# Kernel tuning notes

Measured on AMD Instinct MI355X. Metric: run time of the kernel, lower is better.

The kernel has to match this reference:

```python
import jax, jax.numpy as jnp
import numpy as np

B, Q, G = 32, 4000, 100
C1, C2, C3 = 4, 32, 8
ALPHA, GAMMA = 0.25, 2.0
OTA_K = 5
CENTER_RADIUS = 2.5
COST_BBOX = 1.0
COST_GIOU = 1.0
COST_CLASS = 1.0 / 3.0  # forward sets self.cost_class = 1/len(heads) = 1/3


def box_xyxy_to_cxcywh(b):
    x0, y0, x1, y1 = b[..., 0], b[..., 1], b[..., 2], b[..., 3]
    return jnp.stack([(x0 + x1) * 0.5, (y0 + y1) * 0.5, x1 - x0, y1 - y0], axis=-1)


def box_cxcywh_to_xyxy(b):
    cx, cy, w, h = b[..., 0], b[..., 1], b[..., 2], b[..., 3]
    return jnp.stack([cx - 0.5 * w, cy - 0.5 * h, cx + 0.5 * w, cy + 0.5 * h], axis=-1)


def box_iou(a, b):
    # a [Q,4], b [G,4] in xyxy -> iou, union [Q,G]
    area_a = (a[:, 2] - a[:, 0]) * (a[:, 3] - a[:, 1])
    area_b = (b[:, 2] - b[:, 0]) * (b[:, 3] - b[:, 1])
    lt = jnp.maximum(a[:, None, :2], b[None, :, :2])
    rb = jnp.minimum(a[:, None, 2:], b[None, :, 2:])
    wh = jnp.clip(rb - lt, 0.0)
    inter = wh[..., 0] * wh[..., 1]
    union = area_a[:, None] + area_b[None, :] - inter
    return inter / union, union


def generalized_box_iou(a, b):
    iou, union = box_iou(a, b)
    lt = jnp.minimum(a[:, None, :2], b[None, :, :2])
    rb = jnp.maximum(a[:, None, 2:], b[None, :, 2:])
    wh = jnp.clip(rb - lt, 0.0)
    area = wh[..., 0] * wh[..., 1]
    return iou - (area - union) / area


def get_in_boxes_info(boxes_c, gts_c):
    # boxes_c [Q,4] cxcywh anchors, gts_c [G,4] cxcywh gts
    xy = box_cxcywh_to_xyxy(gts_c)  # [G,4]
    ax, ay = boxes_c[:, 0:1], boxes_c[:, 1:2]  # [Q,1]
    in_box = (ax > xy[:, 0]) & (ax < xy[:, 2]) & (ay > xy[:, 1]) & (ay < xy[:, 3])  # [Q,G]
    w = xy[:, 2] - xy[:, 0]
    h = xy[:, 3] - xy[:, 1]
    cx, cy = gts_c[:, 0], gts_c[:, 1]
    in_ctr = ((ax > cx - CENTER_RADIUS * w) & (ax < cx + CENTER_RADIUS * w) &
              (ay > cy - CENTER_RADIUS * h) & (ay < cy + CENTER_RADIUS * h))
    fg_mask = jnp.any(in_box, axis=1) | jnp.any(in_ctr, axis=1)  # [Q]
    return fg_mask, in_box & in_ctr


def compute_cost(l1, l2, l3, pb, gb, isz, t1, t2, t3):
    fg_mask, in_bc = get_in_boxes_info(box_xyxy_to_cxcywh(pb), box_xyxy_to_cxcywh(gb))
    ious, _ = box_iou(pb, gb)

    def focal_cost(logits, labels):
        p = jax.nn.sigmoid(logits)
        neg = (1.0 - ALPHA) * p ** GAMMA * (-jnp.log(1.0 - p + 1e-8))
        pos = ALPHA * (1.0 - p) ** GAMMA * (-jnp.log(p + 1e-8))
        return (pos - neg)[:, labels]  # [Q,G]

    cc = focal_cost(l1, t1) + focal_cost(l2, t2) + focal_cost(l3, t3)
    nb = pb / isz[None, :]
    ng = gb / isz[None, :]
    cost_bbox = jnp.sum(jnp.abs(nb[:, None, :] - ng[None, :, :]), axis=-1)  # L1 cdist [Q,G]
    cost_giou = -generalized_box_iou(pb, gb)
    cost = (COST_BBOX * cost_bbox + COST_CLASS * cc + COST_GIOU * cost_giou
            + 100.0 * (~in_bc).astype(cost_bbox.dtype))
    cost = cost + 10000.0 * (~fg_mask)[:, None].astype(cost.dtype)
    return cost, ious


def dynamic_k_matching(cost, ious):
    q, g = cost.shape
    topk_ious, _ = jax.lax.top_k(ious.T, OTA_K)  # [G,k]
    dynamic_ks = jnp.clip(topk_ious.sum(1).astype(jnp.int32), 1, None)  # [G]
    # top dynamic_ks[g] lowest-cost queries per gt (dynamic_ks <= OTA_K since ious in [0,1])
    _, pos_idx = jax.lax.top_k(-cost.T, OTA_K)  # [G,k]
    valid = (jnp.arange(OTA_K)[None, :] < dynamic_ks[:, None]).astype(cost.dtype)
    m = jnp.zeros_like(cost).at[pos_idx, jnp.arange(g)[:, None]].add(valid)

    def resolve(m_, c_):
        # anchors matched to >1 gt keep only their min-cost gt
        multi = m_.sum(1) > 1
        one = jax.nn.one_hot(jnp.argmin(c_, axis=1), g, dtype=m_.dtype)
        return jnp.where(multi[:, None], one, m_)

    m = resolve(m, cost)

    def cond(st):
        return jnp.any(st[0].sum(0) == 0)

    def body(st):
        m_, c_ = st
        c_ = c_ + jnp.where((m_.sum(1) > 0)[:, None], 1e5, 0.0)  # penalize already-matched queries
        unmatched = m_.sum(0) == 0  # [G]
        one = jax.nn.one_hot(jnp.argmin(c_, axis=0), q, dtype=m_.dtype, axis=0)  # [Q,G]
        m_ = jnp.where(unmatched[None, :], one, m_)
        m_ = resolve(m_, c_)
        return (m_, c_)

    m, c = jax.lax.while_loop(cond, body, (m, cost))
    selected = m.sum(1) > 0            # [Q] bool: which queries are matched
    gt_idx = jnp.argmax(m, axis=1)     # [Q] gt index per query (valid where selected)
    matched_qidx = jnp.argmin(jnp.where(m > 0, c, jnp.inf), axis=0)  # [G]
    return m, selected, gt_idx, matched_qidx


def reference(pred_logits_1, pred_logits_2, pred_logits_3, pred_boxes, gt_boxes_xyxy, img_size, labels_1, labels_2, labels_3):
    def per_image(l1, l2, l3, pb, gb, isz, t1, t2, t3):
        cost, ious = compute_cost(l1, l2, l3, pb, gb, isz, t1, t2, t3)
        m, selected, gt_idx, matched_qidx = dynamic_k_matching(cost, ious)
        return m, selected, gt_idx, matched_qidx, cost
    return jax.vmap(per_image)(pred_logits_1, pred_logits_2, pred_logits_3,
                               pred_boxes, gt_boxes_xyxy, img_size,
                               labels_1, labels_2, labels_3)


def setup_inputs() -> dict:
    key = jax.random.key(0)
    ks = jax.random.split(key, 8)

    def rand_boxes(k, n):
        k1, k2 = jax.random.split(k)
        cxcy = jax.random.uniform(k1, (B, n, 2), minval=32.0, maxval=480.0)
        wh = jax.random.uniform(k2, (B, n, 2), minval=16.0, maxval=128.0)
        return jnp.concatenate([cxcy - wh * 0.5, cxcy + wh * 0.5], axis=-1)

    return {
        "pred_logits_1": jax.random.normal(ks[0], (B, Q, C1), jnp.float32),
        "pred_logits_2": jax.random.normal(ks[1], (B, Q, C2), jnp.float32),
        "pred_logits_3": jax.random.normal(ks[2], (B, Q, C3), jnp.float32),
        "pred_boxes": rand_boxes(ks[3], Q),
        "gt_boxes_xyxy": rand_boxes(ks[4], G),
        "img_size": jnp.full((B, 4), 512.0, jnp.float32),
        "labels_1": jax.random.randint(ks[5], (B, G), 0, C1),
        "labels_2": jax.random.randint(ks[6], (B, G), 0, C2),
        "labels_3": jax.random.randint(ks[7], (B, G), 0, C3),
    }
```

## Files before the change

### kernel.cpp

```cpp
#include <hip/hip_runtime.h>
#include <math.h>
#include <stdint.h>

#define NB 32
#define NQ 4000
#define NG 100
#define NC1 4
#define NC2 32
#define NC3 8
#define NCT 44
#define GCH 25
#define SLK 16

static const size_t OFF_M    = 0;
static const size_t OFF_SEL  = (size_t)NB * NQ * NG;
static const size_t OFF_GTI  = OFF_SEL + (size_t)NB * NQ;
static const size_t OFF_MQ   = OFF_GTI + (size_t)NB * NQ;
static const size_t OFF_COST = OFF_MQ + (size_t)NB * NG;

__device__ __forceinline__ float focal_diff(float x) {
    float p   = 1.0f / (1.0f + expf(-x));
    float neg = 0.75f * (p * p) * (-logf(1.0f - p + 1e-8f));
    float pos = 0.25f * ((1.0f - p) * (1.0f - p)) * (-logf(p + 1e-8f));
    return pos - neg;
}

__device__ __forceinline__ unsigned ordered_bits(float f) {
    unsigned u = __float_as_uint(f);
    return (u & 0x80000000u) ? ~u : (u | 0x80000000u);
}

__global__ __launch_bounds__(256) void focal_kernel(
    const float* __restrict__ l1, const float* __restrict__ l2, const float* __restrict__ l3,
    float* __restrict__ FDT)
{
    const int b  = blockIdx.y;
    const int q0 = blockIdx.x * 64;
    const int tid = threadIdx.x;
    __shared__ float tile[64][NCT + 1];

    for (int idx = tid; idx < 64 * NC1; idx += 256) {
        const int qi = idx >> 2, c = idx & 3;
        const int q = q0 + qi;
        if (q < NQ) tile[qi][c] = focal_diff(l1[((size_t)b * NQ + q) * NC1 + c]);
    }
    for (int idx = tid; idx < 64 * NC2; idx += 256) {
        const int qi = idx >> 5, c = idx & 31;
        const int q = q0 + qi;
        if (q < NQ) tile[qi][NC1 + c] = focal_diff(l2[((size_t)b * NQ + q) * NC2 + c]);
    }
    for (int idx = tid; idx < 64 * NC3; idx += 256) {
        const int qi = idx >> 3, c = idx & 7;
        const int q = q0 + qi;
        if (q < NQ) tile[qi][NC1 + NC2 + c] = focal_diff(l3[((size_t)b * NQ + q) * NC3 + c]);
    }
    __syncthreads();

    for (int idx = tid; idx < NCT * 64; idx += 256) {
        const int c = idx >> 6, qi = idx & 63;
        const int q = q0 + qi;
        if (q < NQ) FDT[((size_t)b * NCT + c) * NQ + q] = tile[qi][c];
    }
}

__global__ __launch_bounds__(256) void mask_kernel(
    const float* __restrict__ pb, const float* __restrict__ gbx,
    uint4* __restrict__ bmout, float* __restrict__ fgout)
{
    const int b   = blockIdx.y;
    const int tid = threadIdx.x;

    __shared__ float s_ib[NG][4];
    __shared__ float s_ic[NG][4];

    if (tid < NG) {
        const int g = tid;
        const float x0 = gbx[((size_t)b * NG + g) * 4 + 0];
        const float y0 = gbx[((size_t)b * NG + g) * 4 + 1];
        const float x1 = gbx[((size_t)b * NG + g) * 4 + 2];
        const float y1 = gbx[((size_t)b * NG + g) * 4 + 3];
        const float cx = (x0 + x1) * 0.5f, cy = (y0 + y1) * 0.5f;
        const float w0 = x1 - x0, h0 = y1 - y0;
        const float bx0 = cx - 0.5f * w0, bx1 = cx + 0.5f * w0;
        const float by0 = cy - 0.5f * h0, by1 = cy + 0.5f * h0;
        s_ib[g][0] = bx0; s_ib[g][1] = by0; s_ib[g][2] = bx1; s_ib[g][3] = by1;
        const float w = bx1 - bx0, h = by1 - by0;
        s_ic[g][0] = cx - 2.5f * w; s_ic[g][1] = cx + 2.5f * w;
        s_ic[g][2] = cy - 2.5f * h; s_ic[g][3] = cy + 2.5f * h;
    }
    __syncthreads();

    const int q = blockIdx.x * 256 + tid;
    if (q >= NQ) return;

    const float4 pv = reinterpret_cast<const float4*>(pb)[(size_t)b * NQ + q];
    const float ax = (pv.x + pv.z) * 0.5f, ay = (pv.y + pv.w) * 0.5f;

    unsigned bm[4] = {0u, 0u, 0u, 0u};
    bool fg = false;
    for (int g = 0; g < NG; ++g) {
        const bool ib = (ax > s_ib[g][0]) && (ax < s_ib[g][2]) && (ay > s_ib[g][1]) && (ay < s_ib[g][3]);
        const bool ic = (ax > s_ic[g][0]) && (ax < s_ic[g][1]) && (ay > s_ic[g][2]) && (ay < s_ic[g][3]);
        fg = fg || ib || ic;
        if (ib && ic) bm[g >> 5] |= (1u << (g & 31));
    }
    bmout[(size_t)b * NQ + q] = make_uint4(bm[0], bm[1], bm[2], bm[3]);
    fgout[(size_t)b * NQ + q] = fg ? 0.0f : 10000.0f;
}

__global__ __launch_bounds__(256) void cost_kernel(
    const float* __restrict__ pb, const float* __restrict__ gbx, const float* __restrict__ img,
    const int* __restrict__ t1, const int* __restrict__ t2, const int* __restrict__ t3,
    const float* __restrict__ FDT, const uint4* __restrict__ bmin, const float* __restrict__ fgin,
    float* __restrict__ costT)
{
    const int b   = blockIdx.y;
    const int g0  = blockIdx.z * GCH;
    const int tid = threadIdx.x;

    __shared__ float s_ng[GCH][4];
    __shared__ float s_gx[GCH][4];
    __shared__ float s_ab[GCH];
    __shared__ int   s_lab[GCH][3];
    __shared__ float s_isz[4];

    if (tid < 4) s_isz[tid] = img[b * 4 + tid];
    if (tid < GCH) {
        const int g = g0 + tid;
        const float x0 = gbx[((size_t)b * NG + g) * 4 + 0];
        const float y0 = gbx[((size_t)b * NG + g) * 4 + 1];
        const float x1 = gbx[((size_t)b * NG + g) * 4 + 2];
        const float y1 = gbx[((size_t)b * NG + g) * 4 + 3];
        s_gx[tid][0] = x0; s_gx[tid][1] = y0; s_gx[tid][2] = x1; s_gx[tid][3] = y1;
        s_ab[tid] = (x1 - x0) * (y1 - y0);
        s_ng[tid][0] = x0 / img[b * 4 + 0];
        s_ng[tid][1] = y0 / img[b * 4 + 1];
        s_ng[tid][2] = x1 / img[b * 4 + 2];
        s_ng[tid][3] = y1 / img[b * 4 + 3];
        s_lab[tid][0] = t1[b * NG + g];
        s_lab[tid][1] = NC1 + t2[b * NG + g];
        s_lab[tid][2] = NC1 + NC2 + t3[b * NG + g];
    }
    __syncthreads();

    const int q = blockIdx.x * 256 + tid;
    if (q >= NQ) return;

    const float4 pv = reinterpret_cast<const float4*>(pb)[(size_t)b * NQ + q];
    const float p0 = pv.x, p1 = pv.y, p2 = pv.z, p3 = pv.w;
    const float areaA = (p2 - p0) * (p3 - p1);
    const float n0 = p0 / s_isz[0], n1 = p1 / s_isz[1], n2 = p2 / s_isz[2], n3 = p3 / s_isz[3];

    const uint4 bm4 = bmin[(size_t)b * NQ + q];
    const unsigned bm[4] = {bm4.x, bm4.y, bm4.z, bm4.w};
    const float fgadd = fgin[(size_t)b * NQ + q];

    const float* F = FDT + (size_t)b * NCT * NQ + q;
    float* ct = costT + (size_t)b * NG * NQ + q + (size_t)g0 * NQ;
#pragma unroll 5
    for (int gl = 0; gl < GCH; ++gl) {
        const int g = g0 + gl;
        const float f1 = F[(size_t)s_lab[gl][0] * NQ];
        const float f2 = F[(size_t)s_lab[gl][1] * NQ];
        const float f3 = F[(size_t)s_lab[gl][2] * NQ];
        float cb = fabsf(n0 - s_ng[gl][0]);
        cb = cb + fabsf(n1 - s_ng[gl][1]);
        cb = cb + fabsf(n2 - s_ng[gl][2]);
        cb = cb + fabsf(n3 - s_ng[gl][3]);
        const float gx0 = s_gx[gl][0], gy0 = s_gx[gl][1], gx1 = s_gx[gl][2], gy1 = s_gx[gl][3];
        const float ltx = fmaxf(p0, gx0), lty = fmaxf(p1, gy0);
        const float rbx = fminf(p2, gx1), rby = fminf(p3, gy1);
        const float iw = fmaxf(rbx - ltx, 0.0f), ih = fmaxf(rby - lty, 0.0f);
        const float inter = iw * ih;
        const float uni = areaA + s_ab[gl] - inter;
        const float iou = inter / uni;
        const float ex0 = fminf(p0, gx0), ey0 = fminf(p1, gy0);
        const float ex1 = fmaxf(p2, gx1), ey1 = fmaxf(p3, gy1);
        const float ew = fmaxf(ex1 - ex0, 0.0f), eh = fmaxf(ey1 - ey0, 0.0f);
        const float ea = ew * eh;
        const float giou = iou - (ea - uni) / ea;
        const float cc = (f1 + f2) + f3;
        const bool inbc = (bm[g >> 5] >> (g & 31)) & 1u;
        float cost = cb;
        cost = cost + 0.33333334f * cc;
        cost = cost + (-giou);
        cost = cost + (inbc ? 0.0f : 100.0f);
        cost = cost + fgadd;
        ct[(size_t)gl * NQ] = cost;
    }
}

template <bool MAXSEL>
__device__ __forceinline__ bool better(float av, int ai, float bv, int bi) {
    if (MAXSEL) return (av > bv) || (av == bv && ai < bi);
    else        return (av < bv) || (av == bv && ai < bi);
}

template <bool MAXSEL>
__device__ __forceinline__ void ins5(float (&v)[5], int (&id)[5], float nv, int ni) {
    if (!better<MAXSEL>(nv, ni, v[4], id[4])) return;
    v[4] = nv; id[4] = ni;
#pragma unroll
    for (int j = 4; j > 0; --j) {
        if (better<MAXSEL>(v[j], id[j], v[j - 1], id[j - 1])) {
            float tv = v[j]; v[j] = v[j - 1]; v[j - 1] = tv;
            int   ti = id[j]; id[j] = id[j - 1]; id[j - 1] = ti;
        }
    }
}

template <bool MAXSEL>
__device__ __forceinline__ void merge5(float (&v)[5], int (&id)[5], float (&ov)[5], int (&oi)[5]) {
#pragma unroll
    for (int r = 0; r < 5; ++r) {
        float bv = v[0]; int bi = id[0];
#pragma unroll
        for (int off = 32; off >= 1; off >>= 1) {
            float xv = __shfl_xor(bv, off, 64);
            int   xi = __shfl_xor(bi, off, 64);
            if (better<MAXSEL>(xv, xi, bv, bi)) { bv = xv; bi = xi; }
        }
        ov[r] = bv; oi[r] = bi;
        if (id[0] == bi) {
            v[0] = v[1]; id[0] = id[1];
            v[1] = v[2]; id[1] = id[2];
            v[2] = v[3]; id[2] = id[3];
            v[3] = v[4]; id[3] = id[4];
            v[4] = MAXSEL ? -INFINITY : INFINITY; id[4] = 0x7fffffff;
        }
    }
}

__device__ __forceinline__ void push_max5i(float (&v)[5], int (&id)[5], float t, int it) {
#pragma unroll
    for (int i = 0; i < 5; ++i) {
        const bool b = t > v[i];
        const float nv = b ? t : v[i];
        const float nt = b ? v[i] : t;
        const int ni  = b ? it : id[i];
        const int nit = b ? id[i] : it;
        v[i] = nv; id[i] = ni; t = nt; it = nit;
    }
}

#define CHUNK 1000

#define CE(i, j) { const unsigned long long _a = kk[i], _b = kk[j]; \
                   const bool _s = _b < _a; \
                   kk[i] = _s ? _b : _a; kk[j] = _s ? _a : _b; }

__global__ __launch_bounds__(256) void col_topk_kernel(
    const float* __restrict__ pb, const float* __restrict__ gbx, const float* __restrict__ costT,
    int* __restrict__ grc, int* __restrict__ grnew, int* __restrict__ grsl)
{
    const int g = blockIdx.x, b = blockIdx.y;
    const int tid = threadIdx.x, lane = tid & 63, wave = tid >> 6;

    __shared__ float              s_v[4][5];
    __shared__ int                s_i[4][5];
    __shared__ unsigned long long s_ck[4][SLK];

    const float gx0 = gbx[((size_t)b * NG + g) * 4 + 0];
    const float gy0 = gbx[((size_t)b * NG + g) * 4 + 1];
    const float gx1 = gbx[((size_t)b * NG + g) * 4 + 2];
    const float gy1 = gbx[((size_t)b * NG + g) * 4 + 3];
    const float areaB = (gx1 - gx0) * (gy1 - gy0);
    const float4* PB = reinterpret_cast<const float4*>(pb) + (size_t)b * NQ;
    const float* CT = costT + (size_t)b * NG * NQ + (size_t)g * NQ;

    const int q0 = wave * CHUNK, q1 = q0 + CHUNK;

    float cv[16];
#pragma unroll
    for (int i = 0; i < 16; ++i) {
        const bool live = (i < 15) || (lane < 40);
        cv[i] = live ? CT[q0 + i * 64 + lane] : 0.0f;
    }

    {
        float tv[5]; int ti[5];
#pragma unroll
        for (int k = 0; k < 5; ++k) { tv[k] = -INFINITY; ti[k] = 0x7fffffff; }
        for (int base = q0; base < q1; base += 64) {
            const int q = base + lane;
            if (q < q1) {
                const float4 p = PB[q];
                const float ltx = fmaxf(p.x, gx0), lty = fmaxf(p.y, gy0);
                const float rbx = fminf(p.z, gx1), rby = fminf(p.w, gy1);
                const float iw = fmaxf(rbx - ltx, 0.0f), ih = fmaxf(rby - lty, 0.0f);
                const float inter = iw * ih;
                const float areaA = (p.z - p.x) * (p.w - p.y);
                const float uni = areaA + areaB - inter;
                push_max5i(tv, ti, inter / uni, q);
            }
        }
        float ov[5]; int oi[5];
        merge5<true>(tv, ti, ov, oi);
        if (lane == 0) {
#pragma unroll
            for (int k = 0; k < 5; ++k) { s_v[wave][k] = ov[k]; s_i[wave][k] = oi[k]; }
        }
    }

    {
        unsigned long long kk[16];
#pragma unroll
        for (int i = 0; i < 16; ++i) {
            const bool live = (i < 15) || (lane < 40);
            kk[i] = live ? ((((unsigned long long)ordered_bits(cv[i])) << 32)
                            | (unsigned)(q0 + i * 64 + lane))
                         : ~0ull;
        }

        CE(0,1)  CE(2,3)  CE(4,5)  CE(6,7)  CE(8,9)  CE(10,11) CE(12,13) CE(14,15)
        CE(0,2)  CE(1,3)  CE(4,6)  CE(5,7)  CE(8,10) CE(9,11)  CE(12,14) CE(13,15)
        CE(1,2)  CE(5,6)  CE(9,10) CE(13,14)
        CE(0,4)  CE(1,5)  CE(2,6)  CE(3,7)  CE(8,12) CE(9,13)  CE(10,14) CE(11,15)
        CE(2,4)  CE(3,5)  CE(10,12) CE(11,13)
        CE(1,2)  CE(3,4)  CE(5,6)  CE(9,10) CE(11,12) CE(13,14)
        CE(0,8)  CE(1,9)  CE(2,10) CE(3,11) CE(4,12)  CE(5,13)  CE(6,14)  CE(7,15)
        CE(4,8)  CE(5,9)  CE(6,10) CE(7,11)
        CE(2,4)  CE(3,5)  CE(6,8)  CE(7,9)  CE(10,12) CE(11,13)
        CE(1,2)  CE(3,4)  CE(5,6)  CE(7,8)  CE(9,10)  CE(11,12) CE(13,14)

        for (int r = 0; r < SLK; ++r) {
            unsigned long long bk = kk[0];
#pragma unroll
            for (int off = 32; off >= 1; off >>= 1) {
                const unsigned long long xk = __shfl_xor(bk, off, 64);
                if (xk < bk) bk = xk;
            }
            if (lane == 0) s_ck[wave][r] = bk;
            if (kk[0] == bk) {
#pragma unroll
                for (int j = 0; j < 15; ++j) kk[j] = kk[j + 1];
                kk[15] = ~0ull;
            }
        }
    }
    __syncthreads();

    if (tid == 0) {
        float tv[5]; int ti[5];
#pragma unroll
        for (int k = 0; k < 5; ++k) { tv[k] = -INFINITY; ti[k] = 0x7fffffff; }
        for (int w = 0; w < 4; ++w)
#pragma unroll
            for (int k = 0; k < 5; ++k) ins5<true>(tv, ti, s_v[w][k], s_i[w][k]);
        const float s = ((((tv[0] + tv[1]) + tv[2]) + tv[3]) + tv[4]);
        int dk = (int)s;
        if (dk < 1) dk = 1;

        int h0 = 0, h1 = 0, h2 = 0, h3 = 0;
        int* SL = grsl + ((size_t)b * NG + g) * SLK;
        for (int k = 0; k < SLK; ++k) {
            unsigned long long bk = ~0ull; int bw = 0;
            if (h0 < SLK && s_ck[0][h0] < bk) { bk = s_ck[0][h0]; bw = 0; }
            if (h1 < SLK && s_ck[1][h1] < bk) { bk = s_ck[1][h1]; bw = 1; }
            if (h2 < SLK && s_ck[2][h2] < bk) { bk = s_ck[2][h2]; bw = 2; }
            if (h3 < SLK && s_ck[3][h3] < bk) { bk = s_ck[3][h3]; bw = 3; }
            if (bw == 0) h0++; else if (bw == 1) h1++; else if (bw == 2) h2++; else h3++;
            const int bi = (int)(unsigned)(bk & 0xffffffffull);
            SL[k] = bi;
            if (k < dk) {
                atomicAdd(&grc[b * NQ + bi], 1);
                grnew[b * NQ + bi] = g;
            }
        }
    }
}

__device__ __forceinline__ float pen_add(float v, int k) {
    while (k-- > 0) v += 100000.0f;
    return v;
}

__global__ __launch_bounds__(1024) void match_kernel(
    const float* __restrict__ costT, const int* __restrict__ grc, const int* __restrict__ grnew,
    const int* __restrict__ grsl,
    float* __restrict__ out, int* __restrict__ rm_out)
{
    const int b = blockIdx.x, tid = threadIdx.x;
    const int lane = tid & 63, wave = tid >> 6;

    __shared__ short              rmatch[NQ];
    __shared__ short              rnew[NQ];
    __shared__ unsigned short     pen[NQ];
    __shared__ int                rc[NQ];
    __shared__ int                colc[NG];
    __shared__ unsigned long long colkey[NG];
    __shared__ short              sl[NG * SLK];
    __shared__ int                flag;

    const float* CT = costT + (size_t)b * NG * NQ;

    for (int q = tid; q < NQ; q += 1024) {
        rmatch[q] = -1;
        pen[q] = 0;
        rc[q] = grc[b * NQ + q];
        rnew[q] = (short)grnew[b * NQ + q];
    }
    for (int i = tid; i < NG * SLK; i += 1024) sl[i] = (short)grsl[(size_t)b * NG * SLK + i];
    __syncthreads();

    for (int iter = 0; iter < 2000; ++iter) {
        for (int q = tid; q < NQ; q += 1024) {
            const int oldm = rmatch[q];
            const int rcq  = rc[q];
            const int c    = rcq + (oldm >= 0 ? 1 : 0);
            int nm;
            if (c == 0) nm = -1;
            else if (c == 1) nm = rcq ? (int)rnew[q] : oldm;
            else {
                const int kp = pen[q];
                float bv = INFINITY; nm = 0;
                for (int g = 0; g < NG; ++g) {
                    const float v = pen_add(CT[(size_t)g * NQ + q], kp);
                    if (v < bv) { bv = v; nm = g; }
                }
            }
            rmatch[q] = (short)nm; rc[q] = 0;
        }
        __syncthreads();
        if (tid < NG) colc[tid] = 0;
        if (tid == 0) flag = 0;
        __syncthreads();
        for (int q = tid; q < NQ; q += 1024) { const int m = rmatch[q]; if (m >= 0) atomicAdd(&colc[m], 1); }
        __syncthreads();
        if (tid < NG && colc[tid] == 0) flag = 1;
        __syncthreads();
        if (!flag) break;

        for (int q = tid; q < NQ; q += 1024) { if (rmatch[q] >= 0) pen[q]++; }
        __syncthreads();
        for (int g = wave; g < NG; g += 16) {
            if (colc[g] != 0) continue;
            int cand = -1;
            if (lane < SLK) {
                const int qq = (int)sl[g * SLK + lane];
                if (pen[qq] == 0) cand = qq;
            }
            const unsigned long long bal = __ballot(cand >= 0);
            if (bal != 0ull) {
                const int src = __ffsll(bal) - 1;
                const int bi = __shfl(cand, src, 64);
                if (lane == 0) { atomicAdd(&rc[bi], 1); rnew[bi] = (short)g; }
            } else {
                float bv = INFINITY; int bi = 0x7fffffff;
                for (int base = 0; base < NQ; base += 64) {
                    const int q = base + lane;
                    if (q < NQ) {
                        const float v = pen_add(CT[(size_t)g * NQ + q], (int)pen[q]);
                        if (v < bv || (v == bv && q < bi)) { bv = v; bi = q; }
                    }
                }
#pragma unroll
                for (int off = 32; off >= 1; off >>= 1) {
                    const float xv = __shfl_xor(bv, off, 64);
                    const int   xi = __shfl_xor(bi, off, 64);
                    if (xv < bv || (xv == bv && xi < bi)) { bv = xv; bi = xi; }
                }
                if (lane == 0) { atomicAdd(&rc[bi], 1); rnew[bi] = (short)g; }
            }
        }
        __syncthreads();
    }

    if (tid < NG) colkey[tid] = ~0ull;
    __syncthreads();
    for (int q = tid; q < NQ; q += 1024) {
        const int m = rmatch[q];
        out[OFF_SEL + (size_t)b * NQ + q] = (m >= 0) ? 1.0f : 0.0f;
        out[OFF_GTI + (size_t)b * NQ + q] = (float)(m >= 0 ? m : 0);
        rm_out[b * NQ + q] = m;
        if (m >= 0) {
            const float v = pen_add(CT[(size_t)m * NQ + q], (int)pen[q]);
            const unsigned long long key = ((unsigned long long)ordered_bits(v) << 32) | (unsigned)q;
            atomicMin(&colkey[m], key);
        }
    }
    __syncthreads();
    if (tid < NG) out[OFF_MQ + (size_t)b * NG + tid] = (float)(unsigned)(colkey[tid] & 0xffffffffull);
}

__global__ __launch_bounds__(256) void write_out_kernel(
    const float* __restrict__ costT, const int* __restrict__ rm, float* __restrict__ out)
{
    const int b  = blockIdx.y;
    const int q0 = blockIdx.x * 64;
    __shared__ float tile[NG][65];
    __shared__ short srm[64];
    const float* CT = costT + (size_t)b * NG * NQ;
    for (int idx = threadIdx.x; idx < NG * 64; idx += 256) {
        const int g = idx >> 6, qi = idx & 63;
        const int q = q0 + qi;
        if (q < NQ) tile[g][qi] = CT[(size_t)g * NQ + q];
    }
    if (threadIdx.x < 64) {
        const int q = q0 + threadIdx.x;
        srm[threadIdx.x] = (q < NQ) ? (short)rm[b * NQ + q] : (short)-1;
    }
    __syncthreads();
    float* OC = out + OFF_COST + (size_t)b * NQ * NG;
    float* OM = out + OFF_M    + (size_t)b * NQ * NG;
    for (int idx = threadIdx.x; idx < 64 * NG; idx += 256) {
        const int qi = idx / NG, g = idx - qi * NG;
        const int q = q0 + qi;
        if (q < NQ) {
            OC[(size_t)q * NG + g] = tile[g][qi];
            OM[(size_t)q * NG + g] = (srm[qi] == g) ? 1.0f : 0.0f;
        }
    }
}

extern "C" void kernel_launch(void* const* d_in, const int* in_sizes, int n_in,
                              void* d_out, int out_size, void* d_ws, size_t ws_size,
                              hipStream_t stream)
{
    const float* l1  = (const float*)d_in[0];
    const float* l2  = (const float*)d_in[1];
    const float* l3  = (const float*)d_in[2];
    const float* pb  = (const float*)d_in[3];
    const float* gbx = (const float*)d_in[4];
    const float* img = (const float*)d_in[5];
    const int*   t1  = (const int*)d_in[6];
    const int*   t2  = (const int*)d_in[7];
    const int*   t3  = (const int*)d_in[8];
    float* out = (float*)d_out;

    char* ws = (char*)d_ws;
    float* costT = (float*)ws;                                   ws += (size_t)NB * NG * NQ * sizeof(float);
    int*   rm    = (int*)ws;                                     ws += (size_t)NB * NQ * sizeof(int);
    int*   grc   = (int*)ws;                                     ws += (size_t)NB * NQ * sizeof(int);
    int*   grnew = (int*)ws;                                     ws += (size_t)NB * NQ * sizeof(int);
    uint4* bmws  = (uint4*)ws;                                   ws += (size_t)NB * NQ * sizeof(uint4);
    float* fgws  = (float*)ws;                                   ws += (size_t)NB * NQ * sizeof(float);
    int*   grsl  = (int*)ws;

    float* FDT = out + OFF_COST;

    hipMemsetAsync(grc, 0, (size_t)NB * NQ * sizeof(int), stream);

    dim3 fg((NQ + 63) / 64, NB);
    focal_kernel<<<fg, 256, 0, stream>>>(l1, l2, l3, FDT);

    dim3 mk((NQ + 255) / 256, NB);
    mask_kernel<<<mk, 256, 0, stream>>>(pb, gbx, bmws, fgws);

    dim3 cg((NQ + 255) / 256, NB, 4);
    cost_kernel<<<cg, 256, 0, stream>>>(pb, gbx, img, t1, t2, t3, FDT, bmws, fgws, costT);

    dim3 kg(NG, NB);
    col_topk_kernel<<<kg, 256, 0, stream>>>(pb, gbx, costT, grc, grnew, grsl);

    match_kernel<<<NB, 1024, 0, stream>>>(costT, grc, grnew, grsl, out, rm);

    dim3 wg((NQ + 63) / 64, NB);
    write_out_kernel<<<wg, 256, 0, stream>>>(costT, rm, out);
}
```

Measured before the change: 335.1 us.

## Use worklists and incremental column counts in iterative matching loop

The per-iteration full scans over all 4000 queries are replaced by a double-buffered worklist holding only the queries that received a new request. Column counts are updated incrementally with atomics instead of being recounted each iteration, and the per-query penalty array is replaced by a matched-since timestamp from which the penalty is derived. This removes several full-array passes and barriers per iteration. The cost is more shared-memory atomics and a fixed worklist capacity of 1024 entries, which could overflow if the initial request count exceeds it.

After: 314.3 us. 6.2% less time.

```diff
diff --git a/kernel.cpp b/kernel.cpp
--- a/kernel.cpp
+++ b/kernel.cpp
@@ -385,72 +385,84 @@
 
     __shared__ short              rmatch[NQ];
     __shared__ short              rnew[NQ];
-    __shared__ unsigned short     pen[NQ];
+    __shared__ short              tmat[NQ];
     __shared__ int                rc[NQ];
     __shared__ int                colc[NG];
     __shared__ unsigned long long colkey[NG];
     __shared__ short              sl[NG * SLK];
-    __shared__ int                flag;
+    __shared__ short              zlist[NG];
+    __shared__ short              wl[2][1024];
+    __shared__ int                wlc[2];
+    __shared__ int                zcount;
 
     const float* CT = costT + (size_t)b * NG * NQ;
+
+    if (tid == 0) { wlc[0] = 0; wlc[1] = 0; }
+    if (tid < NG) colc[tid] = 0;
+    __syncthreads();
 
     for (int q = tid; q < NQ; q += 1024) {
         rmatch[q] = -1;
-        pen[q] = 0;
-        rc[q] = grc[b * NQ + q];
+        const int r = grc[b * NQ + q];
+        rc[q] = r;
         rnew[q] = (short)grnew[b * NQ + q];
+        if (r > 0) { const int i = atomicAdd(&wlc[0], 1); wl[0][i] = (short)q; }
     }
     for (int i = tid; i < NG * SLK; i += 1024) sl[i] = (short)grsl[(size_t)b * NG * SLK + i];
     __syncthreads();
 
+    int L = 2000;
     for (int iter = 0; iter < 2000; ++iter) {
-        for (int q = tid; q < NQ; q += 1024) {
+        const int p = iter & 1;
+        const int n = wlc[p];
+        for (int i = tid; i < n; i += 1024) {
+            const int q = (int)wl[p][i];
+            const int rcq = atomicExch(&rc[q], 0);
+            if (rcq == 0) continue;
             const int oldm = rmatch[q];
-            const int rcq  = rc[q];
-            const int c    = rcq + (oldm >= 0 ? 1 : 0);
+            const int c = rcq + (oldm >= 0 ? 1 : 0);
             int nm;
-            if (c == 0) nm = -1;
-            else if (c == 1) nm = rcq ? (int)rnew[q] : oldm;
+            if (c == 1) nm = (int)rnew[q];
             else {
-                const int kp = pen[q];
+                const int kp = (oldm >= 0) ? (iter - (int)tmat[q]) : 0;
                 float bv = INFINITY; nm = 0;
                 for (int g = 0; g < NG; ++g) {
                     const float v = pen_add(CT[(size_t)g * NQ + q], kp);
                     if (v < bv) { bv = v; nm = g; }
                 }
             }
-            rmatch[q] = (short)nm; rc[q] = 0;
-        }
+            rmatch[q] = (short)nm;
+            if (oldm < 0) { tmat[q] = (short)iter; atomicAdd(&colc[nm], 1); }
+            else if (oldm != nm) { atomicSub(&colc[oldm], 1); atomicAdd(&colc[nm], 1); }
+        }
+        if (tid == 0) { wlc[p ^ 1] = 0; zcount = 0; }
         __syncthreads();
-        if (tid < NG) colc[tid] = 0;
-        if (tid == 0) flag = 0;
+
+        if (tid < NG && colc[tid] == 0) { const int i = atomicAdd(&zcount, 1); zlist[i] = (short)tid; }
         __syncthreads();
-        for (int q = tid; q < NQ; q += 1024) { const int m = rmatch[q]; if (m >= 0) atomicAdd(&colc[m], 1); }
-        __syncthreads();
-        if (tid < NG && colc[tid] == 0) flag = 1;
-        __syncthreads();
-        if (!flag) break;
-
-        for (int q = tid; q < NQ; q += 1024) { if (rmatch[q] >= 0) pen[q]++; }
-        __syncthreads();
-        for (int g = wave; g < NG; g += 16) {
-            if (colc[g] != 0) continue;
+
+        const int zn = zcount;
+        if (zn == 0) { L = iter; break; }
+
+        for (int zi = wave; zi < zn; zi += 16) {
+            const int g = (int)zlist[zi];
             int cand = -1;
             if (lane < SLK) {
                 const int qq = (int)sl[g * SLK + lane];
-                if (pen[qq] == 0) cand = qq;
+                if (rmatch[qq] < 0) cand = qq;
             }
             const unsigned long long bal = __ballot(cand >= 0);
+            int bi;
             if (bal != 0ull) {
                 const int src = __ffsll(bal) - 1;
-                const int bi = __shfl(cand, src, 64);
-                if (lane == 0) { atomicAdd(&rc[bi], 1); rnew[bi] = (short)g; }
+                bi = __shfl(cand, src, 64);
             } else {
-                float bv = INFINITY; int bi = 0x7fffffff;
+                float bv = INFINITY; bi = 0x7fffffff;
                 for (int base = 0; base < NQ; base += 64) {
                     const int q = base + lane;
                     if (q < NQ) {
-                        const float v = pen_add(CT[(size_t)g * NQ + q], (int)pen[q]);
+                        const int kp = (rmatch[q] >= 0) ? (iter + 1 - (int)tmat[q]) : 0;
+                        const float v = pen_add(CT[(size_t)g * NQ + q], kp);
                         if (v < bv || (v == bv && q < bi)) { bv = v; bi = q; }
                     }
                 }
@@ -460,7 +472,12 @@
                     const int   xi = __shfl_xor(bi, off, 64);
                     if (xv < bv || (xv == bv && xi < bi)) { bv = xv; bi = xi; }
                 }
-                if (lane == 0) { atomicAdd(&rc[bi], 1); rnew[bi] = (short)g; }
+            }
+            if (lane == 0) {
+                atomicAdd(&rc[bi], 1);
+                rnew[bi] = (short)g;
+                const int i = atomicAdd(&wlc[p ^ 1], 1);
+                wl[p ^ 1][i] = (short)bi;
             }
         }
         __syncthreads();
@@ -474,7 +491,7 @@
         out[OFF_GTI + (size_t)b * NQ + q] = (float)(m >= 0 ? m : 0);
         rm_out[b * NQ + q] = m;
         if (m >= 0) {
-            const float v = pen_add(CT[(size_t)m * NQ + q], (int)pen[q]);
+            const float v = pen_add(CT[(size_t)m * NQ + q], L - (int)tmat[q]);
             const unsigned long long key = ((unsigned long long)ordered_bits(v) << 32) | (unsigned)q;
             atomicMin(&colkey[m], key);
         }
```
